# Kernel tuning notes

Hardware: AMD Instinct MI355X
Metric: run time of the kernel (lower is better)

## Reference

```python
import jax, jax.numpy as jnp
import numpy as np

N, E, IN, HID, H, C, L, NC = 10000, 60000, 768, 256, 8, 256, 4, 2
EPS, SLOPE = 1e-5, 0.2

def _ln(x, g, b):
    m = x.mean(-1, keepdims=True)
    v = x.var(-1, keepdims=True)
    return (x - m) / jnp.sqrt(v + EPS) * g + b

def _gelu(x):
    return jax.nn.gelu(x, approximate=False)  # torch nn.GELU default (erf)

def setup_inputs() -> dict:
    key = jax.random.key(0)
    ks = iter(jax.random.split(key, 40))
    def p(shape, s=0.02):
        return jax.random.normal(next(ks), shape, jnp.float32) * s
    return dict(
        x=jax.random.normal(next(ks), (N, IN), jnp.float32),
        edge_index=jax.random.randint(next(ks), (2, E), 0, N, dtype=jnp.int32),
        W_in=p((HID, IN)), b_in=jnp.zeros((HID,), jnp.float32),
        virtual_node=p((1, HID)),
        Wl=p((L, H * C, HID)), bl=jnp.zeros((L, H * C), jnp.float32),
        Wr=p((L, H * C, HID)), br=jnp.zeros((L, H * C), jnp.float32),
        att=p((L, H, C)), gbias=jnp.zeros((L, HID), jnp.float32),
        V1=p((L, 2 * HID, HID)), v1b=jnp.zeros((L, 2 * HID), jnp.float32),
        V2=p((L, HID, 2 * HID)), v2b=jnp.zeros((L, HID), jnp.float32),
        U1=p((L, 2 * HID, 2 * HID)), u1b=jnp.zeros((L, 2 * HID), jnp.float32),
        U2=p((L, HID, 2 * HID)), u2b=jnp.zeros((L, HID), jnp.float32),
        g1=jnp.ones((L, HID), jnp.float32), be1=jnp.zeros((L, HID), jnp.float32),
        g2=jnp.ones((L, HID), jnp.float32), be2=jnp.zeros((L, HID), jnp.float32),
        g3=jnp.ones((L, HID), jnp.float32), be3=jnp.zeros((L, HID), jnp.float32),
        O1=p((HID, HID)), o1b=jnp.zeros((HID,), jnp.float32),
        O2=p((NC, HID)), o2b=jnp.zeros((NC,), jnp.float32),
    )

def reference(x, edge_index, W_in, b_in, virtual_node, Wl, bl, Wr, br, att, gbias,
              V1, v1b, V2, v2b, U1, u1b, U2, u2b,
              g1, be1, g2, be2, g3, be3, O1, o1b, O2, o2b):
    # add self loops (PyG add_self_loops=True)
    loops = jnp.arange(N, dtype=edge_index.dtype)
    src = jnp.concatenate([edge_index[0], loops])  # message sources j
    dst = jnp.concatenate([edge_index[1], loops])  # message targets i

    x = x @ W_in.T + b_in                      # [N, HID]
    vn = virtual_node                          # [1, HID]
    for i in range(L):
        # --- GATv2Conv (concat=False -> mean over heads), eval mode (no dropout) ---
        xl = (x @ Wl[i].T + bl[i]).reshape(N, H, C)   # source transform
        xr = (x @ Wr[i].T + br[i]).reshape(N, H, C)   # target transform
        m = jax.nn.leaky_relu(xl[src] + xr[dst], SLOPE)       # [Etot, H, C]
        e = jnp.einsum('ehc,hc->eh', m, att[i])                # [Etot, H]
        emax = jax.ops.segment_max(e, dst, num_segments=N)
        a = jnp.exp(e - emax[dst])
        denom = jax.ops.segment_sum(a, dst, num_segments=N)
        alpha = a / denom[dst]                                  # segment softmax
        agg = jax.ops.segment_sum(xl[src] * alpha[:, :, None], dst, num_segments=N)
        x_local = agg.mean(axis=1) + gbias[i]                   # [N, HID]
        x = _ln(x + x_local, g1[i], be1[i])
        # --- virtual node update ---
        vn_in = x.mean(axis=0, keepdims=True)
        vn_up = _gelu(vn_in @ V1[i].T + v1b[i]) @ V2[i].T + v2b[i]
        vn = _ln(vn + vn_up, g2[i], be2[i])
        # --- node update with broadcast VN ---
        xc = jnp.concatenate([x, jnp.broadcast_to(vn, (N, HID))], axis=1)
        xu = _gelu(xc @ U1[i].T + u1b[i]) @ U2[i].T + u2b[i]
        x = _ln(x + xu, g3[i], be3[i])
    return _gelu(x @ O1.T + o1b) @ O2.T + o2b
```

## Files before the change

kernel.cpp:

```cpp
#include <hip/hip_runtime.h>
#include <hip/hip_bf16.h>
#include <cstdint>
#include <cstddef>

#define N_NODES 10000
#define M_PAD   10112
#define N_EDGES 60000
#define ETOT    70000
#define DIM_IN  768
#define HID     256
#define NHEAD   8
#define CH      256
#define HC      2048
#define NLAYER  4
#define NCLS    2
#define EPSLN   1e-5f
#define SLOPE   0.2f
#define DEG_CAP 128

typedef __bf16 bf16;
typedef __bf16 bf16x8 __attribute__((ext_vector_type(8)));
typedef float  f32x4  __attribute__((ext_vector_type(4)));

__device__ __forceinline__ float gelu_erf(float x) {
  return 0.5f * x * (1.0f + erff(x * 0.70710678118654752f));
}

__device__ __forceinline__ void gl2lds16(const void* g, void* l) {
  __builtin_amdgcn_global_load_lds(
      (const __attribute__((address_space(1))) unsigned int*)g,
      (__attribute__((address_space(3))) unsigned int*)l,
      16, 0, 0);
}

__global__ void k_count(const int* __restrict__ ei, int* __restrict__ deg) {
  int e = blockIdx.x * 256 + threadIdx.x;
  if (e >= ETOT) return;
  int d = (e < N_EDGES) ? ei[N_EDGES + e] : (e - N_EDGES);
  atomicAdd(&deg[d], 1);
}

__global__ void k_scan(const int* __restrict__ deg, int* __restrict__ offs) {
  __shared__ int lds[1024];
  const int t = threadIdx.x;
  const int c0 = t * 10;
  int s = 0;
  #pragma unroll
  for (int q = 0; q < 10; ++q) { int idx = c0 + q; if (idx < N_NODES) s += deg[idx]; }
  lds[t] = s;
  __syncthreads();
  for (int o = 1; o < 1024; o <<= 1) {
    int v = (t >= o) ? lds[t - o] : 0;
    __syncthreads();
    lds[t] += v;
    __syncthreads();
  }
  int run = lds[t] - s;
  #pragma unroll
  for (int q = 0; q < 10; ++q) {
    int idx = c0 + q;
    if (idx < N_NODES) { offs[idx] = run; run += deg[idx]; }
  }
  if (t == 1023) offs[N_NODES] = lds[1023];
}

__global__ void k_scatter(const int* __restrict__ ei, const int* __restrict__ offs,
                          int* __restrict__ fill, int* __restrict__ adj) {
  int e = blockIdx.x * 256 + threadIdx.x;
  if (e >= ETOT) return;
  int s, d;
  if (e < N_EDGES) { s = ei[e]; d = ei[N_EDGES + e]; } else { s = e - N_EDGES; d = s; }
  int pos = offs[d] + atomicAdd(&fill[d], 1);
  adj[pos] = s;
}

__global__ void k_init_vn(const float* __restrict__ vnode, float* __restrict__ vn_cur) {
  int t = threadIdx.x;
  if (t < HID) vn_cur[t] = vnode[t];
}

__global__ void k_f2b(const float* __restrict__ src, bf16* __restrict__ dst, int n4) {
  int i = blockIdx.x * 256 + threadIdx.x;
  int stride = gridDim.x * 256;
  for (; i < n4; i += stride) {
    float4 v = reinterpret_cast<const float4*>(src)[i];
    bf16 o0 = (bf16)v.x, o1 = (bf16)v.y, o2 = (bf16)v.z, o3 = (bf16)v.w;
    ushort4 pack;
    pack.x = __builtin_bit_cast(unsigned short, o0);
    pack.y = __builtin_bit_cast(unsigned short, o1);
    pack.z = __builtin_bit_cast(unsigned short, o2);
    pack.w = __builtin_bit_cast(unsigned short, o3);
    reinterpret_cast<ushort4*>(dst)[i] = pack;
  }
}

__global__ void k_catw(const float* __restrict__ Wl, const float* __restrict__ Wr,
                       bf16* __restrict__ out) {
  int idx = blockIdx.x * 256 + threadIdx.x;
  const int total8 = NLAYER * 4096 * 256 / 8;
  if (idx >= total8) return;
  size_t flat = (size_t)idx * 8;
  int i   = (int)(flat / (4096 * 256));
  int rem = (int)(flat % (4096 * 256));
  int r = rem >> 8;
  int k = rem & 255;
  const float* src = (r < 2048)
      ? Wl + (((size_t)i * 2048 + r) << 8) + k
      : Wr + (((size_t)i * 2048 + (r - 2048)) << 8) + k;
  const float4* p4 = reinterpret_cast<const float4*>(src);
  float4 u0 = p4[0], u1 = p4[1];
  bf16x8 ov;
  ov[0]=(bf16)u0.x; ov[1]=(bf16)u0.y; ov[2]=(bf16)u0.z; ov[3]=(bf16)u0.w;
  ov[4]=(bf16)u1.x; ov[5]=(bf16)u1.y; ov[6]=(bf16)u1.z; ov[7]=(bf16)u1.w;
  reinterpret_cast<bf16x8*>(out)[idx] = ov;
}

__global__ void k_catb(const float* __restrict__ bl, const float* __restrict__ br,
                       float* __restrict__ out) {
  int idx = blockIdx.x * 256 + threadIdx.x;
  if (idx >= NLAYER * 4096) return;
  int i = idx >> 12, r = idx & 4095;
  out[idx] = (r < 2048) ? bl[i * 2048 + r] : br[i * 2048 + (r - 2048)];
}

template<int ACT, bool WB, bool WF>
__global__ __launch_bounds__(256) void k_gemm2(
    const bf16* __restrict__ A, int lda,
    const bf16* __restrict__ W, int ldw,
    const float* __restrict__ bias,
    bf16* __restrict__ Cb, float* __restrict__ Cf, int ldc,
    int M, int K, int NT)
{
  __shared__ bf16 As[2][128 * 64];
  __shared__ bf16 Bs[2][128 * 64];
  const int t = threadIdx.x;
  const int nwg = gridDim.x;
  const int qq = nwg >> 3, rr = nwg & 7;
  const int xcd = blockIdx.x & 7, loc = blockIdx.x >> 3;
  const int wg = (xcd < rr) ? (xcd * (qq + 1) + loc)
                            : (rr * (qq + 1) + (xcd - rr) * qq + loc);
  const int bm = (wg / NT) * 128;
  const int bn = (wg % NT) * 128;
  const int l = t & 63, w = t >> 6;
  const int wm = (w >> 1) * 64, wn = (w & 1) * 64;
  const int lr = l & 15, lg = l >> 4;
  const int sr = t >> 3;
  const int ps = t & 7;

  f32x4 acc[4][4];
  #pragma unroll
  for (int a = 0; a < 4; ++a)
    #pragma unroll
    for (int b = 0; b < 4; ++b) acc[a][b] = (f32x4){0.f, 0.f, 0.f, 0.f};

  auto stage = [&](int buf, int k0) {
    #pragma unroll
    for (int q = 0; q < 4; ++q) {
      int r = q * 32 + sr;
      int ls = ps ^ (r & 7);
      gl2lds16(A + (size_t)(bm + r) * lda + k0 + ls * 8, &As[buf][r * 64 + ps * 8]);
    }
    #pragma unroll
    for (int q = 0; q < 4; ++q) {
      int r = q * 32 + sr;
      int ls = ps ^ (r & 7);
      gl2lds16(W + (size_t)(bn + r) * ldw + k0 + ls * 8, &Bs[buf][r * 64 + ps * 8]);
    }
  };

  const int nt = K >> 6;
  stage(0, 0);
  __syncthreads();
  for (int kt = 0; kt < nt; ++kt) {
    if (kt + 1 < nt) stage((kt + 1) & 1, (kt + 1) << 6);
    const bf16* Ab = As[kt & 1];
    const bf16* Bb = Bs[kt & 1];
    #pragma unroll
    for (int ks = 0; ks < 2; ++ks) {
      bf16x8 af[4], bfr[4];
      #pragma unroll
      for (int mt = 0; mt < 4; ++mt) {
        int row = wm + mt * 16 + lr;
        int slot = ks * 4 + lg;
        af[mt] = *reinterpret_cast<const bf16x8*>(&Ab[row * 64 + ((slot ^ (row & 7)) * 8)]);
      }
      #pragma unroll
      for (int nt2 = 0; nt2 < 4; ++nt2) {
        int row = wn + nt2 * 16 + lr;
        int slot = ks * 4 + lg;
        bfr[nt2] = *reinterpret_cast<const bf16x8*>(&Bb[row * 64 + ((slot ^ (row & 7)) * 8)]);
      }
      #pragma unroll
      for (int mt = 0; mt < 4; ++mt)
        #pragma unroll
        for (int nt2 = 0; nt2 < 4; ++nt2)
          acc[mt][nt2] = __builtin_amdgcn_mfma_f32_16x16x32_bf16(af[mt], bfr[nt2], acc[mt][nt2], 0, 0, 0);
    }
    __syncthreads();
  }
  #pragma unroll
  for (int mt = 0; mt < 4; ++mt) {
    #pragma unroll
    for (int nt2 = 0; nt2 < 4; ++nt2) {
      int col = bn + wn + nt2 * 16 + lr;
      float bv = bias[col];
      #pragma unroll
      for (int j = 0; j < 4; ++j) {
        int row = bm + wm + mt * 16 + lg * 4 + j;
        if (row < M) {
          float vv = acc[mt][nt2][j] + bv;
          if (ACT == 1) vv = gelu_erf(vv);
          if (WB) Cb[(size_t)row * ldc + col] = (bf16)vv;
          if (WF) Cf[(size_t)row * ldc + col] = vv;
        }
      }
    }
  }
}

__global__ __launch_bounds__(256) void k_node_attn(
    float* __restrict__ x, bf16* __restrict__ xb,
    const bf16* __restrict__ xlr,
    const int* __restrict__ offs, const int* __restrict__ adj,
    const float* __restrict__ att_l, const float* __restrict__ gbias_l,
    const float* __restrict__ g_l, const float* __restrict__ b_l)
{
  __shared__ int   s_src[DEG_CAP];
  __shared__ float s_agg[HC];
  __shared__ float s_red[8];

  const int t = threadIdx.x;
  const int i = blockIdx.x;
  const int start = offs[i];
  int deg = offs[i + 1] - start;
  if (deg > DEG_CAP) deg = DEG_CAP;

  for (int j = t; j < deg; j += 256) s_src[j] = adj[start + j];

  float xr_reg[8], att_reg[8];
  {
    bf16x8 xv = *reinterpret_cast<const bf16x8*>(xlr + (size_t)i * 4096 + 2048 + 8 * t);
    #pragma unroll
    for (int q = 0; q < 8; ++q) xr_reg[q] = (float)xv[q];
    const float4* ap = reinterpret_cast<const float4*>(att_l + 8 * t);
    float4 a0 = ap[0], a1 = ap[1];
    att_reg[0]=a0.x; att_reg[1]=a0.y; att_reg[2]=a0.z; att_reg[3]=a0.w;
    att_reg[4]=a1.x; att_reg[5]=a1.y; att_reg[6]=a1.z; att_reg[7]=a1.w;
  }
  __syncthreads();

  float m = -1e30f, ssum = 0.f;
  float acc[8];
  #pragma unroll
  for (int q = 0; q < 8; ++q) acc[q] = 0.f;

  for (int j = 0; j < deg; ++j) {
    bf16x8 xv = *reinterpret_cast<const bf16x8*>(xlr + (size_t)s_src[j] * 4096 + 8 * t);
    float xf[8];
    float p = 0.f;
    #pragma unroll
    for (int q = 0; q < 8; ++q) {
      xf[q] = (float)xv[q];
      float z = xf[q] + xr_reg[q];
      z = (z > 0.f) ? z : SLOPE * z;
      p = fmaf(att_reg[q], z, p);
    }
    #pragma unroll
    for (int o = 16; o >= 1; o >>= 1) p += __shfl_xor(p, o, 32);
    if (__any(p > m)) {
      float mn = fmaxf(m, p);
      float scale = __expf(m - mn);
      ssum *= scale;
      #pragma unroll
      for (int q = 0; q < 8; ++q) acc[q] *= scale;
      m = mn;
    }
    float a = __expf(p - m);
    ssum += a;
    #pragma unroll
    for (int q = 0; q < 8; ++q) acc[q] = fmaf(a, xf[q], acc[q]);
  }
  float inv = 1.0f / ssum;
  #pragma unroll
  for (int q = 0; q < 8; ++q) s_agg[8 * t + q] = acc[q] * inv;
  __syncthreads();

  float xloc = 0.f;
  #pragma unroll
  for (int hh = 0; hh < NHEAD; ++hh) xloc += s_agg[hh * CH + t];
  xloc = xloc * (1.0f / NHEAD) + gbias_l[t];
  float r = x[(size_t)i * HID + t] + xloc;

  float s1 = r, s2 = r * r;
  #pragma unroll
  for (int o = 32; o >= 1; o >>= 1) { s1 += __shfl_xor(s1, o); s2 += __shfl_xor(s2, o); }
  if ((t & 63) == 0) { s_red[t >> 6] = s1; s_red[4 + (t >> 6)] = s2; }
  __syncthreads();
  s1 = s_red[0] + s_red[1] + s_red[2] + s_red[3];
  s2 = s_red[4] + s_red[5] + s_red[6] + s_red[7];
  float mean = s1 * (1.0f / HID);
  float var  = s2 * (1.0f / HID) - mean * mean;
  float o = (r - mean) * rsqrtf(var + EPSLN) * g_l[t] + b_l[t];
  x [(size_t)i * HID + t] = o;
  xb[(size_t)i * HID + t] = (bf16)o;
}

__global__ void k_colmean(const float* __restrict__ x, float* __restrict__ accum) {
  const int t = threadIdx.x, b = blockIdx.x;
  float s = 0.f;
  for (int r = b * 50; r < (b + 1) * 50; ++r) s += x[(size_t)r * HID + t];
  atomicAdd(&accum[t], s);
}

__global__ void k_vn_gemv1(const float* __restrict__ vn_accum,
                           const float* __restrict__ V1, const float* __restrict__ v1b,
                           float* __restrict__ z1) {
  const int o = blockIdx.x * 8 + (threadIdx.x >> 5);
  const int lane = threadIdx.x & 31;
  const float4* vp = reinterpret_cast<const float4*>(vn_accum + lane * 8);
  float4 a0 = vp[0], a1 = vp[1];
  const float4* wp = reinterpret_cast<const float4*>(V1 + (size_t)o * 256 + lane * 8);
  float4 w0 = wp[0], w1 = wp[1];
  float p = a0.x*w0.x + a0.y*w0.y + a0.z*w0.z + a0.w*w0.w
          + a1.x*w1.x + a1.y*w1.y + a1.z*w1.z + a1.w*w1.w;
  #pragma unroll
  for (int s = 16; s >= 1; s >>= 1) p += __shfl_xor(p, s, 32);
  if (lane == 0) z1[o] = gelu_erf(p * (1.0f / (float)N_NODES) + v1b[o]);
}

__global__ void k_vn_gemv2(const float* __restrict__ z1,
                           const float* __restrict__ V2, const float* __restrict__ v2b,
                           float* __restrict__ vn_up) {
  const int o = blockIdx.x * 8 + (threadIdx.x >> 5);
  const int lane = threadIdx.x & 31;
  float p = 0.f;
  #pragma unroll
  for (int c = 0; c < 4; ++c) {
    float4 a = reinterpret_cast<const float4*>(z1 + lane * 16)[c];
    float4 w = reinterpret_cast<const float4*>(V2 + (size_t)o * 512 + lane * 16)[c];
    p += a.x*w.x + a.y*w.y + a.z*w.z + a.w*w.w;
  }
  #pragma unroll
  for (int s = 16; s >= 1; s >>= 1) p += __shfl_xor(p, s, 32);
  if (lane == 0) vn_up[o] = p + v2b[o];
}

__global__ void k_vn_ln(float* __restrict__ vn_cur, const float* __restrict__ vn_up,
                        const float* __restrict__ g2, const float* __restrict__ be2) {
  __shared__ float s_red[8];
  const int t = threadIdx.x;
  float r = vn_cur[t] + vn_up[t];
  float s1 = r, s2 = r * r;
  #pragma unroll
  for (int o = 32; o >= 1; o >>= 1) { s1 += __shfl_xor(s1, o); s2 += __shfl_xor(s2, o); }
  if ((t & 63) == 0) { s_red[t >> 6] = s1; s_red[4 + (t >> 6)] = s2; }
  __syncthreads();
  s1 = s_red[0] + s_red[1] + s_red[2] + s_red[3];
  s2 = s_red[4] + s_red[5] + s_red[6] + s_red[7];
  float mean = s1 * (1.0f / HID);
  float var  = s2 * (1.0f / HID) - mean * mean;
  vn_cur[t] = (r - mean) * rsqrtf(var + EPSLN) * g2[t] + be2[t];
}

__global__ void k_vn_ctr(const float* __restrict__ vn_cur,
                         const float* __restrict__ U1, const float* __restrict__ u1b,
                         float* __restrict__ vn_ctr) {
  const int o = blockIdx.x * 8 + (threadIdx.x >> 5);
  const int lane = threadIdx.x & 31;
  const float4* vp = reinterpret_cast<const float4*>(vn_cur + lane * 8);
  float4 a0 = vp[0], a1 = vp[1];
  const float4* wp = reinterpret_cast<const float4*>(U1 + (size_t)o * 512 + 256 + lane * 8);
  float4 w0 = wp[0], w1 = wp[1];
  float p = a0.x*w0.x + a0.y*w0.y + a0.z*w0.z + a0.w*w0.w
          + a1.x*w1.x + a1.y*w1.y + a1.z*w1.z + a1.w*w1.w;
  #pragma unroll
  for (int s = 16; s >= 1; s >>= 1) p += __shfl_xor(p, s, 32);
  if (lane == 0) vn_ctr[o] = p + u1b[o];
}

__global__ __launch_bounds__(256) void k_ln_res(
    float* __restrict__ x, bf16* __restrict__ xb, const float* __restrict__ xu,
    const float* __restrict__ g_l, const float* __restrict__ b_l)
{
  __shared__ float s_red[8];
  const int t = threadIdx.x, i = blockIdx.x;
  float r = x[(size_t)i * HID + t] + xu[(size_t)i * HID + t];
  float s1 = r, s2 = r * r;
  #pragma unroll
  for (int o = 32; o >= 1; o >>= 1) { s1 += __shfl_xor(s1, o); s2 += __shfl_xor(s2, o); }
  if ((t & 63) == 0) { s_red[t >> 6] = s1; s_red[4 + (t >> 6)] = s2; }
  __syncthreads();
  s1 = s_red[0] + s_red[1] + s_red[2] + s_red[3];
  s2 = s_red[4] + s_red[5] + s_red[6] + s_red[7];
  float mean = s1 * (1.0f / HID);
  float var  = s2 * (1.0f / HID) - mean * mean;
  float o = (r - mean) * rsqrtf(var + EPSLN) * g_l[t] + b_l[t];
  x [(size_t)i * HID + t] = o;
  xb[(size_t)i * HID + t] = (bf16)o;
}

__global__ void k_final(const float* __restrict__ g, const float* __restrict__ O2,
                        const float* __restrict__ o2b, float* __restrict__ out) {
  int tid = blockIdx.x * 256 + threadIdx.x;
  if (tid >= N_NODES * NCLS) return;
  int n = tid >> 1, j = tid & 1;
  const float* gr = g + (size_t)n * HID;
  const float* w  = O2 + (size_t)j * HID;
  float d = o2b[j];
  for (int k = 0; k < HID; ++k) d = fmaf(gr[k], w[k], d);
  out[tid] = d;
}

extern "C" void kernel_launch(void* const* d_in, const int* in_sizes, int n_in,
                              void* d_out, int out_size, void* d_ws, size_t ws_size,
                              hipStream_t stream)
{
  const float* x_in  = (const float*)d_in[0];
  const int*   ei    = (const int*)  d_in[1];
  const float* W_in  = (const float*)d_in[2];
  const float* b_in  = (const float*)d_in[3];
  const float* vnode = (const float*)d_in[4];
  const float* Wl    = (const float*)d_in[5];
  const float* bl    = (const float*)d_in[6];
  const float* Wr    = (const float*)d_in[7];
  const float* br    = (const float*)d_in[8];
  const float* att   = (const float*)d_in[9];
  const float* gbias = (const float*)d_in[10];
  const float* V1    = (const float*)d_in[11];
  const float* v1b   = (const float*)d_in[12];
  const float* V2    = (const float*)d_in[13];
  const float* v2b   = (const float*)d_in[14];
  const float* U1    = (const float*)d_in[15];
  const float* u1b   = (const float*)d_in[16];
  const float* U2    = (const float*)d_in[17];
  const float* u2b   = (const float*)d_in[18];
  const float* g1    = (const float*)d_in[19];
  const float* be1   = (const float*)d_in[20];
  const float* g2    = (const float*)d_in[21];
  const float* be2   = (const float*)d_in[22];
  const float* g3    = (const float*)d_in[23];
  const float* be3   = (const float*)d_in[24];
  const float* O1    = (const float*)d_in[25];
  const float* o1b   = (const float*)d_in[26];
  const float* O2    = (const float*)d_in[27];
  const float* o2b   = (const float*)d_in[28];
  float* out = (float*)d_out;

  char* ws = (char*)d_ws;
  size_t cur = 0;
  auto alloc = [&](size_t bytes) -> char* {
    char* p = ws + cur;
    cur = (cur + bytes + 255) & ~(size_t)255;
    return p;
  };
  float* x        = (float*)alloc((size_t)M_PAD * HID * 4);
  bf16*  xb       = (bf16*) alloc((size_t)M_PAD * HID * 2);
  bf16*  xlr      = (bf16*) alloc((size_t)M_PAD * 4096 * 2);
  bf16*  h1       = (bf16*) alloc((size_t)M_PAD * 2 * HID * 2);
  float* xu       = (float*)alloc((size_t)M_PAD * HID * 4);
  bf16*  Wlrb     = (bf16*) alloc((size_t)NLAYER * 4096 * HID * 2);
  float* blr      = (float*)alloc((size_t)NLAYER * 4096 * 4);
  bf16*  U1b      = (bf16*) alloc((size_t)NLAYER * 2 * HID * 2 * HID * 2);
  bf16*  U2b      = (bf16*) alloc((size_t)NLAYER * HID * 2 * HID * 2);
  bf16*  O1b      = (bf16*) alloc((size_t)HID * HID * 2);
  bf16*  Winb     = (bf16*) alloc((size_t)HID * DIM_IN * 2);
  int*   deg      = (int*)  alloc((size_t)N_NODES * 4);
  int*   offs     = (int*)  alloc((size_t)(N_NODES + 1) * 4);
  int*   fill     = (int*)  alloc((size_t)N_NODES * 4);
  int*   adj      = (int*)  alloc((size_t)ETOT * 4);
  float* vn_accum = (float*)alloc(HID * 4);
  float* vn_cur   = (float*)alloc(HID * 4);
  float* vn_ctr   = (float*)alloc(2 * HID * 4);
  float* z1buf    = (float*)alloc(2 * HID * 4);
  float* vn_up    = (float*)alloc(HID * 4);

  bf16* x_in_b = xlr;

  hipMemsetAsync(deg, 0, (size_t)N_NODES * 4, stream);
  hipMemsetAsync(fill, 0, (size_t)N_NODES * 4, stream);
  k_count<<<(ETOT + 255) / 256, 256, 0, stream>>>(ei, deg);
  k_scan<<<1, 1024, 0, stream>>>(deg, offs);
  k_scatter<<<(ETOT + 255) / 256, 256, 0, stream>>>(ei, offs, fill, adj);
  k_init_vn<<<1, 256, 0, stream>>>(vnode, vn_cur);

  k_catw<<<(NLAYER * 4096 * 256 / 8 + 255) / 256, 256, 0, stream>>>(Wl, Wr, Wlrb);
  k_catb<<<(NLAYER * 4096 + 255) / 256, 256, 0, stream>>>(bl, br, blr);
  k_f2b<<<256, 256, 0, stream>>>(U1, U1b, NLAYER * 2 * HID * 2 * HID / 4);
  k_f2b<<<128, 256, 0, stream>>>(U2, U2b, NLAYER * HID * 2 * HID / 4);
  k_f2b<<<64, 256, 0, stream>>>(O1, O1b, HID * HID / 4);
  k_f2b<<<64, 256, 0, stream>>>(W_in, Winb, HID * DIM_IN / 4);
  k_f2b<<<512, 256, 0, stream>>>(x_in, x_in_b, N_NODES * DIM_IN / 4);

  const int MT = M_PAD / 128;

  k_gemm2<0, true, true><<<MT * 2, 256, 0, stream>>>(
      x_in_b, DIM_IN, Winb, DIM_IN, b_in, xb, x, HID, N_NODES, DIM_IN, 2);

  for (int i = 0; i < NLAYER; ++i) {
    const bf16* Wlrb_i = Wlrb + (size_t)i * 4096 * HID;
    const bf16* U1b_i  = U1b + (size_t)i * 2 * HID * 2 * HID;
    const bf16* U2b_i  = U2b + (size_t)i * HID * 2 * HID;

    k_gemm2<0, true, false><<<MT * 32, 256, 0, stream>>>(
        xb, HID, Wlrb_i, HID, blr + (size_t)i * 4096, xlr, nullptr, 4096, N_NODES, HID, 32);

    k_node_attn<<<N_NODES, 256, 0, stream>>>(x, xb, xlr, offs, adj,
        att + (size_t)i * HC, gbias + (size_t)i * HID,
        g1 + (size_t)i * HID, be1 + (size_t)i * HID);

    hipMemsetAsync(vn_accum, 0, HID * 4, stream);
    k_colmean<<<200, 256, 0, stream>>>(x, vn_accum);
    k_vn_gemv1<<<64, 256, 0, stream>>>(vn_accum,
        V1 + (size_t)i * 2 * HID * HID, v1b + (size_t)i * 2 * HID, z1buf);
    k_vn_gemv2<<<32, 256, 0, stream>>>(z1buf,
        V2 + (size_t)i * HID * 2 * HID, v2b + (size_t)i * HID, vn_up);
    k_vn_ln<<<1, 256, 0, stream>>>(vn_cur, vn_up,
        g2 + (size_t)i * HID, be2 + (size_t)i * HID);
    k_vn_ctr<<<64, 256, 0, stream>>>(vn_cur,
        U1 + (size_t)i * 2 * HID * 2 * HID, u1b + (size_t)i * 2 * HID, vn_ctr);

    k_gemm2<1, true, false><<<MT * 4, 256, 0, stream>>>(
        xb, HID, U1b_i, 2 * HID, vn_ctr, h1, nullptr, 2 * HID, N_NODES, HID, 4);
    k_gemm2<0, false, true><<<MT * 2, 256, 0, stream>>>(
        h1, 2 * HID, U2b_i, 2 * HID, u2b + (size_t)i * HID, nullptr, xu, HID, N_NODES, 2 * HID, 2);

    k_ln_res<<<N_NODES, 256, 0, stream>>>(x, xb, xu, g3 + (size_t)i * HID, be3 + (size_t)i * HID);
  }

  k_gemm2<1, false, true><<<MT * 2, 256, 0, stream>>>(
      xb, HID, O1b, HID, o1b, nullptr, xu, HID, N_NODES, HID, 2);
  k_final<<<(N_NODES * NCLS + 255) / 256, 256, 0, stream>>>(xu, O2, o2b, out);
}
```

Measured before the change: 971.9 us.

## Halve GEMM K-tile with vmcnt-based pipelining and rewrite leaky-ReLU as abs FMA

The bf16 MFMA GEMM now stages 32-wide K tiles instead of 64, with a matching XOR swizzle. Each iteration uses an explicit s_waitcnt vmcnt plus raw barriers, so the prefetch of the next tile can stay in flight while the current one is consumed. This halves LDS use per block, which may raise occupancy, but doubles the number of barriers per K. Separately, the GATv2 attention score computes leaky-ReLU as 0.6*z + 0.4*|z| with prescaled attention vectors, removing the compare/select.

```diff
diff --git a/kernel.cpp b/kernel.cpp
--- a/kernel.cpp
+++ b/kernel.cpp
@@ -131,8 +131,8 @@
     bf16* __restrict__ Cb, float* __restrict__ Cf, int ldc,
     int M, int K, int NT)
 {
-  __shared__ bf16 As[2][128 * 64];
-  __shared__ bf16 Bs[2][128 * 64];
+  __shared__ bf16 As[2][128 * 32];
+  __shared__ bf16 Bs[2][128 * 32];
   const int t = threadIdx.x;
   const int nwg = gridDim.x;
   const int qq = nwg >> 3, rr = nwg & 7;
@@ -144,8 +144,8 @@
   const int l = t & 63, w = t >> 6;
   const int wm = (w >> 1) * 64, wn = (w & 1) * 64;
   const int lr = l & 15, lg = l >> 4;
-  const int sr = t >> 3;
-  const int ps = t & 7;
+  const int sr = t >> 2;
+  const int ps = t & 3;
 
   f32x4 acc[4][4];
   #pragma unroll
@@ -155,48 +155,51 @@
 
   auto stage = [&](int buf, int k0) {
     #pragma unroll
-    for (int q = 0; q < 4; ++q) {
-      int r = q * 32 + sr;
-      int ls = ps ^ (r & 7);
-      gl2lds16(A + (size_t)(bm + r) * lda + k0 + ls * 8, &As[buf][r * 64 + ps * 8]);
-    }
-    #pragma unroll
-    for (int q = 0; q < 4; ++q) {
-      int r = q * 32 + sr;
-      int ls = ps ^ (r & 7);
-      gl2lds16(W + (size_t)(bn + r) * ldw + k0 + ls * 8, &Bs[buf][r * 64 + ps * 8]);
+    for (int q = 0; q < 2; ++q) {
+      int r = q * 64 + sr;
+      int ls = ps ^ ((r >> 1) & 3);
+      gl2lds16(A + (size_t)(bm + r) * lda + k0 + ls * 8, &As[buf][r * 32 + ps * 8]);
+    }
+    #pragma unroll
+    for (int q = 0; q < 2; ++q) {
+      int r = q * 64 + sr;
+      int ls = ps ^ ((r >> 1) & 3);
+      gl2lds16(W + (size_t)(bn + r) * ldw + k0 + ls * 8, &Bs[buf][r * 32 + ps * 8]);
     }
   };
 
-  const int nt = K >> 6;
+  const int nt = K >> 5;
   stage(0, 0);
-  __syncthreads();
   for (int kt = 0; kt < nt; ++kt) {
-    if (kt + 1 < nt) stage((kt + 1) & 1, (kt + 1) << 6);
+    if (kt + 1 < nt) {
+      stage((kt + 1) & 1, (kt + 1) << 5);
+      asm volatile("s_waitcnt vmcnt(4)" ::: "memory");
+    } else {
+      asm volatile("s_waitcnt vmcnt(0)" ::: "memory");
+    }
+    __builtin_amdgcn_s_barrier();
+    asm volatile("" ::: "memory");
     const bf16* Ab = As[kt & 1];
     const bf16* Bb = Bs[kt & 1];
-    #pragma unroll
-    for (int ks = 0; ks < 2; ++ks) {
-      bf16x8 af[4], bfr[4];
+    bf16x8 af[4], bfr[4];
+    #pragma unroll
+    for (int mt = 0; mt < 4; ++mt) {
+      int row = wm + mt * 16 + lr;
+      af[mt] = *reinterpret_cast<const bf16x8*>(&Ab[row * 32 + ((lg ^ ((row >> 1) & 3)) * 8)]);
+    }
+    #pragma unroll
+    for (int nt2 = 0; nt2 < 4; ++nt2) {
+      int row = wn + nt2 * 16 + lr;
+      bfr[nt2] = *reinterpret_cast<const bf16x8*>(&Bb[row * 32 + ((lg ^ ((row >> 1) & 3)) * 8)]);
+    }
+    #pragma unroll
+    for (int mt = 0; mt < 4; ++mt)
       #pragma unroll
-      for (int mt = 0; mt < 4; ++mt) {
-        int row = wm + mt * 16 + lr;
-        int slot = ks * 4 + lg;
-        af[mt] = *reinterpret_cast<const bf16x8*>(&Ab[row * 64 + ((slot ^ (row & 7)) * 8)]);
-      }
-      #pragma unroll
-      for (int nt2 = 0; nt2 < 4; ++nt2) {
-        int row = wn + nt2 * 16 + lr;
-        int slot = ks * 4 + lg;
-        bfr[nt2] = *reinterpret_cast<const bf16x8*>(&Bb[row * 64 + ((slot ^ (row & 7)) * 8)]);
-      }
-      #pragma unroll
-      for (int mt = 0; mt < 4; ++mt)
-        #pragma unroll
-        for (int nt2 = 0; nt2 < 4; ++nt2)
-          acc[mt][nt2] = __builtin_amdgcn_mfma_f32_16x16x32_bf16(af[mt], bfr[nt2], acc[mt][nt2], 0, 0, 0);
-    }
-    __syncthreads();
+      for (int nt2 = 0; nt2 < 4; ++nt2)
+        acc[mt][nt2] = __builtin_amdgcn_mfma_f32_16x16x32_bf16(af[mt], bfr[nt2], acc[mt][nt2], 0, 0, 0);
+    asm volatile("" ::: "memory");
+    __builtin_amdgcn_s_barrier();
+    asm volatile("" ::: "memory");
   }
   #pragma unroll
   for (int mt = 0; mt < 4; ++mt) {
@@ -237,15 +240,17 @@
 
   for (int j = t; j < deg; j += 256) s_src[j] = adj[start + j];
 
-  float xr_reg[8], att_reg[8];
+  float xr_reg[8], a6[8], a4[8];
   {
     bf16x8 xv = *reinterpret_cast<const bf16x8*>(xlr + (size_t)i * 4096 + 2048 + 8 * t);
     #pragma unroll
     for (int q = 0; q < 8; ++q) xr_reg[q] = (float)xv[q];
     const float4* ap = reinterpret_cast<const float4*>(att_l + 8 * t);
     float4 a0 = ap[0], a1 = ap[1];
-    att_reg[0]=a0.x; att_reg[1]=a0.y; att_reg[2]=a0.z; att_reg[3]=a0.w;
-    att_reg[4]=a1.x; att_reg[5]=a1.y; att_reg[6]=a1.z; att_reg[7]=a1.w;
+    a6[0]=0.6f*a0.x; a6[1]=0.6f*a0.y; a6[2]=0.6f*a0.z; a6[3]=0.6f*a0.w;
+    a6[4]=0.6f*a1.x; a6[5]=0.6f*a1.y; a6[6]=0.6f*a1.z; a6[7]=0.6f*a1.w;
+    a4[0]=0.4f*a0.x; a4[1]=0.4f*a0.y; a4[2]=0.4f*a0.z; a4[3]=0.4f*a0.w;
+    a4[4]=0.4f*a1.x; a4[5]=0.4f*a1.y; a4[6]=0.4f*a1.z; a4[7]=0.4f*a1.w;
   }
   __syncthreads();
 
@@ -262,8 +267,8 @@
     for (int q = 0; q < 8; ++q) {
       xf[q] = (float)xv[q];
       float z = xf[q] + xr_reg[q];
-      z = (z > 0.f) ? z : SLOPE * z;
-      p = fmaf(att_reg[q], z, p);
+      p = fmaf(a6[q], z, p);
+      p = fmaf(a4[q], fabsf(z), p);
     }
     #pragma unroll
     for (int o = 16; o >= 1; o >>= 1) p += __shfl_xor(p, o, 32);
```

New measurement: 1.019 ms. 4.9% more time.
